# Kernel optimization log

Measured on AMD Instinct MI355X. Metric: run time of the kernel, lower is better.

## Reference

```python
import jax, jax.numpy as jnp
import numpy as np
import math

C = 1024
H = 16
D = C // H
R = 4  # max_relative_position (window_size)


def setup_inputs() -> dict:
    key = jax.random.key(0)
    ks = jax.random.split(key, 10)
    B, S = 2, 2048
    scale = 1.0 / math.sqrt(C)
    inp = {
        "x": jax.random.normal(ks[0], (B, S, C), dtype=jnp.float32),
        "mask": jnp.ones((B, 1, 1, S), dtype=jnp.int32),
        "Wq": jax.random.normal(ks[1], (C, C), dtype=jnp.float32) * scale,
        "bq": jnp.zeros((C,), dtype=jnp.float32),
        "Wk": jax.random.normal(ks[2], (C, C), dtype=jnp.float32) * scale,
        "bk": jnp.zeros((C,), dtype=jnp.float32),
        "Wv": jax.random.normal(ks[3], (C, C), dtype=jnp.float32) * scale,
        "bv": jnp.zeros((C,), dtype=jnp.float32),
        "Wo": jax.random.normal(ks[4], (C, C), dtype=jnp.float32) * scale,
        "bo": jnp.zeros((C,), dtype=jnp.float32),
        "rel_key": jax.random.normal(ks[5], (2 * R + 1, D), dtype=jnp.float32) * 0.02,
    }
    return inp


def reference(x, mask, Wq, bq, Wk, bk, Wv, bv, Wo, bo, rel_key):
    B, S, Cc = x.shape
    inv = 1.0 / math.sqrt(D)
    # projections -> [B, H, S, D]
    q = (x @ Wq.T + bq).reshape(B, S, H, D).transpose(0, 2, 1, 3)
    k = (x @ Wk.T + bk).reshape(B, S, H, D).transpose(0, 2, 1, 3)
    v = (x @ Wv.T + bv).reshape(B, S, H, D).transpose(0, 2, 1, 3)
    scores = jnp.einsum("bhqd,bhkd->bhqk", q, k) * inv
    # relative position bias: positions[q,k] in [0, 2R]
    pos = jnp.clip(jnp.arange(S)[None, :] - jnp.arange(S)[:, None], -R, R) + R
    # project q onto the small rel table first ([B,H,S,2R+1]), then gather per (q,k)
    proj = jnp.einsum("bhqd,rd->bhqr", q, rel_key) * inv
    rel_scores = proj[:, :, jnp.arange(S)[:, None], pos]  # [B,H,S,S]
    scores = scores + rel_scores
    scores = jnp.where(mask == 0, jnp.float32(-1e9), scores)
    attn = jax.nn.softmax(scores, axis=-1)
    out = jnp.einsum("bhqk,bhkd->bhqd", attn, v)
    out = out.transpose(0, 2, 1, 3).reshape(B, S, Cc)
    return out @ Wo.T + bo
```

## Files before the change

kernel.cpp:

```cpp
#include <hip/hip_runtime.h>

#define B_ 2
#define S_ 2048
#define C_ 1024
#define H_ 16
#define D_ 64

typedef _Float16 f16;
typedef _Float16 half8 __attribute__((ext_vector_type(8)));
typedef _Float16 half4v __attribute__((ext_vector_type(4)));
typedef float floatx4 __attribute__((ext_vector_type(4)));

#define LD4F(p) (*reinterpret_cast<const float4*>(p))
#define LD16U(p) (*reinterpret_cast<const uint4*>(p))
#define EXP2F(x) __builtin_amdgcn_exp2f(x)

__device__ __forceinline__ void gload16(const f16* g, f16* l) {
    __builtin_amdgcn_global_load_lds(
        (const __attribute__((address_space(1))) void*)g,
        (__attribute__((address_space(3))) void*)l, 16, 0, 0);
}

__global__ __launch_bounds__(256)
void convert_inputs(const float* __restrict__ x,
                    const float* __restrict__ Wq, const float* __restrict__ Wk,
                    const float* __restrict__ Wv, const float* __restrict__ Wo,
                    f16* __restrict__ dst)
{
    const size_t XN = (size_t)B_ * S_ * C_;
    const size_t WN = (size_t)C_ * C_;
    size_t i = (size_t)blockIdx.x * 256 + threadIdx.x;
    size_t e = i * 4;
    if (e >= XN + 4 * WN) return;
    const float* s; size_t o;
    if (e < XN) { s = x; o = e; }
    else {
        size_t j = e - XN;
        int w = (int)(j >> 20);
        s = (w == 0) ? Wq : (w == 1) ? Wk : (w == 2) ? Wv : Wo;
        o = j & (WN - 1);
    }
    float4 val = LD4F(&s[o]);
    half4v hv;
    hv[0] = (f16)val.x; hv[1] = (f16)val.y; hv[2] = (f16)val.z; hv[3] = (f16)val.w;
    *reinterpret_cast<half4v*>(&dst[e]) = hv;
}

__global__ __launch_bounds__(256)
void qkv_gemm_h(const f16* __restrict__ xh, const f16* __restrict__ Wbase,
                const float* __restrict__ bq, const float* __restrict__ bk,
                const float* __restrict__ bv,
                f16* __restrict__ qo, f16* __restrict__ ko, f16* __restrict__ vo)
{
    const int which = blockIdx.z;
    const f16* W      = Wbase + (size_t)which * C_ * C_;
    const float* bias = (which == 0) ? bq : (which == 1) ? bk : bv;
    f16* out          = (which == 0) ? qo : (which == 1) ? ko : vo;
    const float qscale = (which == 0) ? 0.18033688f : 1.0f;

    const int mb = blockIdx.x * 128;
    const int nb = blockIdx.y * 128;
    const int tid = threadIdx.x;
    const int lane = tid & 63;
    const int wid = tid >> 6;
    const int wr = wid >> 1, wc = wid & 1;
    const int l15 = lane & 15, g = lane >> 4;

    __shared__ __align__(16) f16 As[128 * 32];
    __shared__ __align__(16) f16 Bs[128 * 32];

    floatx4 acc[4][4];
#pragma unroll
    for (int m = 0; m < 4; ++m)
#pragma unroll
        for (int n = 0; n < 4; ++n) acc[m][n] = (floatx4){0.f, 0.f, 0.f, 0.f};

    for (int k0 = 0; k0 < C_; k0 += 32) {
        __syncthreads();
#pragma unroll
        for (int p = 0; p < 2; ++p) {
            int i2 = tid + 256 * p;
            int row = i2 >> 2, c4 = i2 & 3;
            gload16(&xh[(size_t)(mb + row) * C_ + k0 + c4 * 8], &As[i2 * 8]);
            gload16(&W [(size_t)(nb + row) * C_ + k0 + c4 * 8], &Bs[i2 * 8]);
        }
        __syncthreads();

        half8 af[4];
#pragma unroll
        for (int m = 0; m < 4; ++m)
            af[m] = *reinterpret_cast<const half8*>(&As[(wr * 64 + m * 16 + l15) * 32 + g * 8]);
#pragma unroll
        for (int n = 0; n < 4; ++n) {
            half8 bf = *reinterpret_cast<const half8*>(&Bs[(wc * 64 + n * 16 + l15) * 32 + g * 8]);
#pragma unroll
            for (int m = 0; m < 4; ++m)
                acc[m][n] = __builtin_amdgcn_mfma_f32_16x16x32_f16(af[m], bf, acc[m][n], 0, 0, 0);
        }
    }

#pragma unroll
    for (int n = 0; n < 4; ++n) {
        int col = nb + wc * 64 + n * 16 + l15;
        float bb = bias[col];
        int h = col >> 6, d = col & 63;
#pragma unroll
        for (int m = 0; m < 4; ++m)
#pragma unroll
            for (int r = 0; r < 4; ++r) {
                int row = mb + wr * 64 + m * 16 + g * 4 + r;
                int b = row >> 11, s = row & (S_ - 1);
                out[(((size_t)b * H_ + h) * S_ + s) * D_ + d] = (f16)((acc[m][n][r] + bb) * qscale);
            }
    }
}

__global__ __launch_bounds__(256)
void attn_mfma(const f16* __restrict__ q, const f16* __restrict__ k,
               const f16* __restrict__ v, const int* __restrict__ mask,
               const float* __restrict__ rel, f16* __restrict__ ctx)
{
    const int flat = blockIdx.y * 32 + blockIdx.x;
    const int c = flat & 7, j = flat >> 3;
    const int bh = (c << 2) | (j >> 5);
    const int qb = (j & 31) * 64;

    const int b = bh >> 4, h = bh & 15;
    const f16* qh_ = q + (size_t)bh * S_ * D_;
    const f16* kh_ = k + (size_t)bh * S_ * D_;
    const f16* vh_ = v + (size_t)bh * S_ * D_;

    const int tid = threadIdx.x;
    const int lane = tid & 63;
    const int wid = tid >> 6;
    const int l15 = lane & 15, g = lane >> 4;

    __shared__ __align__(16) f16 Ks[64 * 72];
    __shared__ __align__(16) f16 Vt[64 * 72];
    __shared__ __align__(16) f16 Ps[4][16 * 72];
    __shared__ float Prj[64][12];

    const int qrow = qb + wid * 16 + l15;
    half8 aq0 = *reinterpret_cast<const half8*>(&qh_[(size_t)qrow * D_ + g * 8]);
    half8 aq1 = *reinterpret_cast<const half8*>(&qh_[(size_t)qrow * D_ + 32 + g * 8]);

#pragma unroll
    for (int rr = 0; rr < 9; ++rr) {
        float p = 0.f;
#pragma unroll
        for (int jj = 0; jj < 8; ++jj) {
            p += (float)aq0[jj] * rel[rr * D_ + g * 8 + jj];
            p += (float)aq1[jj] * rel[rr * D_ + 32 + g * 8 + jj];
        }
        p += __shfl_xor(p, 16);
        p += __shfl_xor(p, 32);
        if (lane < 16) Prj[wid * 16 + l15][rr] = p;
    }

    float prj_lo[4], prj_hi[4];
#pragma unroll
    for (int r = 0; r < 4; ++r) {
        prj_lo[r] = Prj[wid * 16 + g * 4 + r][0];
        prj_hi[r] = Prj[wid * 16 + g * 4 + r][8];
    }

    floatx4 o[4];
    float mrun[4], lrun[4];
#pragma unroll
    for (int n = 0; n < 4; ++n) o[n] = (floatx4){0.f, 0.f, 0.f, 0.f};
#pragma unroll
    for (int r = 0; r < 4; ++r) { mrun[r] = -INFINITY; lrun[r] = 0.f; }

    for (int jt = 0; jt < S_ / 64; ++jt) {
        const int jb = jt * 64;
        uint4 kr[2], vr[2];
#pragma unroll
        for (int p = 0; p < 2; ++p) {
            int idx = tid + 256 * p;
            int row = idx >> 3, c8 = idx & 7;
            kr[p] = LD16U(&kh_[(size_t)(jb + row) * D_ + c8 * 8]);
            vr[p] = LD16U(&vh_[(size_t)(jb + row) * D_ + c8 * 8]);
        }
        __syncthreads();
#pragma unroll
        for (int p = 0; p < 2; ++p) {
            int idx = tid + 256 * p;
            int row = idx >> 3, c8 = idx & 7;
            *reinterpret_cast<uint4*>(&Ks[row * 72 + c8 * 8]) = kr[p];
            const f16* vp = reinterpret_cast<const f16*>(&vr[p]);
#pragma unroll
            for (int jj = 0; jj < 8; ++jj) {
                int dd = (jj + c8) & 7;
                Vt[(c8 * 8 + dd) * 72 + row] = vp[dd];
            }
        }
        __syncthreads();

        floatx4 sc[4];
#pragma unroll
        for (int n = 0; n < 4; ++n) sc[n] = (floatx4){0.f, 0.f, 0.f, 0.f};
#pragma unroll
        for (int n = 0; n < 4; ++n) {
            half8 bk0 = *reinterpret_cast<const half8*>(&Ks[(n * 16 + l15) * 72 + g * 8]);
            half8 bk1 = *reinterpret_cast<const half8*>(&Ks[(n * 16 + l15) * 72 + 32 + g * 8]);
            sc[n] = __builtin_amdgcn_mfma_f32_16x16x32_f16(aq0, bk0, sc[n], 0, 0, 0);
            sc[n] = __builtin_amdgcn_mfma_f32_16x16x32_f16(aq1, bk1, sc[n], 0, 0, 0);
        }

        float pvv[4][4];
        const bool diag = (jb >= qb - 64) && (jb <= qb + 64);
        if (!diag) {
            const float* pb = (jb > qb) ? prj_hi : prj_lo;
#pragma unroll
            for (int n = 0; n < 4; ++n) {
                int mv = mask[b * S_ + jb + n * 16 + l15];
#pragma unroll
                for (int r = 0; r < 4; ++r)
                    pvv[n][r] = mv ? (sc[n][r] + pb[r]) : -1.0e9f;
            }
        } else {
#pragma unroll
            for (int n = 0; n < 4; ++n) {
                int jg = jb + n * 16 + l15;
                int mv = mask[b * S_ + jg];
#pragma unroll
                for (int r = 0; r < 4; ++r) {
                    int ig = qb + wid * 16 + g * 4 + r;
                    int dp = jg - ig;
                    dp = dp < -4 ? -4 : (dp > 4 ? 4 : dp);
                    float val = sc[n][r] + Prj[wid * 16 + g * 4 + r][dp + 4];
                    pvv[n][r] = mv ? val : -1.0e9f;
                }
            }
        }

#pragma unroll
        for (int r = 0; r < 4; ++r) {
            float mx = fmaxf(fmaxf(pvv[0][r], pvv[1][r]), fmaxf(pvv[2][r], pvv[3][r]));
            mx = fmaxf(mx, __shfl_xor(mx, 1));
            mx = fmaxf(mx, __shfl_xor(mx, 2));
            mx = fmaxf(mx, __shfl_xor(mx, 4));
            mx = fmaxf(mx, __shfl_xor(mx, 8));
            float mnew = fmaxf(mrun[r], mx);
            float scl = EXP2F(mrun[r] - mnew);
            float rs = 0.f;
#pragma unroll
            for (int n = 0; n < 4; ++n) {
                float e = EXP2F(pvv[n][r] - mnew);
                pvv[n][r] = e; rs += e;
            }
            rs += __shfl_xor(rs, 1); rs += __shfl_xor(rs, 2);
            rs += __shfl_xor(rs, 4); rs += __shfl_xor(rs, 8);
            lrun[r] = lrun[r] * scl + rs;
            mrun[r] = mnew;
#pragma unroll
            for (int n = 0; n < 4; ++n) o[n][r] *= scl;
        }

#pragma unroll
        for (int n = 0; n < 4; ++n)
#pragma unroll
            for (int r = 0; r < 4; ++r)
                Ps[wid][(g * 4 + r) * 72 + n * 16 + l15] = (f16)pvv[n][r];

        half8 pa0 = *reinterpret_cast<const half8*>(&Ps[wid][l15 * 72 + g * 8]);
        half8 pa1 = *reinterpret_cast<const half8*>(&Ps[wid][l15 * 72 + 32 + g * 8]);

#pragma unroll
        for (int n = 0; n < 4; ++n) {
            half8 bv0 = *reinterpret_cast<const half8*>(&Vt[(n * 16 + l15) * 72 + g * 8]);
            half8 bv1 = *reinterpret_cast<const half8*>(&Vt[(n * 16 + l15) * 72 + 32 + g * 8]);
            o[n] = __builtin_amdgcn_mfma_f32_16x16x32_f16(pa0, bv0, o[n], 0, 0, 0);
            o[n] = __builtin_amdgcn_mfma_f32_16x16x32_f16(pa1, bv1, o[n], 0, 0, 0);
        }
    }

#pragma unroll
    for (int n = 0; n < 4; ++n) {
        int dcol = n * 16 + l15;
#pragma unroll
        for (int r = 0; r < 4; ++r) {
            int srow = qb + wid * 16 + g * 4 + r;
            float val = o[n][r] / lrun[r];
            ctx[((size_t)(b * S_ + srow)) * C_ + h * D_ + dcol] = (f16)val;
        }
    }
}

__global__ __launch_bounds__(256)
void out_gemm_h(const f16* __restrict__ A, const f16* __restrict__ W,
                const float* __restrict__ bias, float* __restrict__ out)
{
    const int mb = blockIdx.x * 128;
    const int nb = blockIdx.y * 128;
    const int tid = threadIdx.x;
    const int lane = tid & 63;
    const int wid = tid >> 6;
    const int wr = wid >> 1, wc = wid & 1;
    const int l15 = lane & 15, g = lane >> 4;

    __shared__ __align__(16) f16 As[128 * 32];
    __shared__ __align__(16) f16 Bs[128 * 32];

    floatx4 acc[4][4];
#pragma unroll
    for (int m = 0; m < 4; ++m)
#pragma unroll
        for (int n = 0; n < 4; ++n) acc[m][n] = (floatx4){0.f, 0.f, 0.f, 0.f};

    for (int k0 = 0; k0 < C_; k0 += 32) {
        __syncthreads();
#pragma unroll
        for (int p = 0; p < 2; ++p) {
            int i2 = tid + 256 * p;
            int row = i2 >> 2, c4 = i2 & 3;
            gload16(&A[(size_t)(mb + row) * C_ + k0 + c4 * 8], &As[i2 * 8]);
            gload16(&W[(size_t)(nb + row) * C_ + k0 + c4 * 8], &Bs[i2 * 8]);
        }
        __syncthreads();

        half8 af[4];
#pragma unroll
        for (int m = 0; m < 4; ++m)
            af[m] = *reinterpret_cast<const half8*>(&As[(wr * 64 + m * 16 + l15) * 32 + g * 8]);
#pragma unroll
        for (int n = 0; n < 4; ++n) {
            half8 bf = *reinterpret_cast<const half8*>(&Bs[(wc * 64 + n * 16 + l15) * 32 + g * 8]);
#pragma unroll
            for (int m = 0; m < 4; ++m)
                acc[m][n] = __builtin_amdgcn_mfma_f32_16x16x32_f16(af[m], bf, acc[m][n], 0, 0, 0);
        }
    }

#pragma unroll
    for (int n = 0; n < 4; ++n) {
        int col = nb + wc * 64 + n * 16 + l15;
        float bb = bias[col];
#pragma unroll
        for (int m = 0; m < 4; ++m)
#pragma unroll
            for (int r = 0; r < 4; ++r) {
                size_t row = mb + wr * 64 + m * 16 + g * 4 + r;
                out[row * C_ + col] = acc[m][n][r] + bb;
            }
    }
}

extern "C" void kernel_launch(void* const* d_in, const int* in_sizes, int n_in,
                              void* d_out, int out_size, void* d_ws, size_t ws_size,
                              hipStream_t stream)
{
    const float* x    = (const float*)d_in[0];
    const int*   mask = (const int*)  d_in[1];
    const float* Wq   = (const float*)d_in[2];
    const float* bq   = (const float*)d_in[3];
    const float* Wk   = (const float*)d_in[4];
    const float* bk   = (const float*)d_in[5];
    const float* Wv   = (const float*)d_in[6];
    const float* bv   = (const float*)d_in[7];
    const float* Wo   = (const float*)d_in[8];
    const float* bo   = (const float*)d_in[9];
    const float* rel  = (const float*)d_in[10];
    float* out = (float*)d_out;

    const size_t XN = (size_t)B_ * S_ * C_;
    const size_t WN = (size_t)C_ * C_;

    f16* wsh  = (f16*)d_ws;
    f16* xh   = wsh;
    f16* Wqh  = wsh + XN;
    f16* Woh  = Wqh + 3 * WN;
    f16* qh   = wsh + XN + 4 * WN;
    f16* kh   = qh + XN;
    f16* vh   = kh + XN;
    f16* ctxh = vh + XN;

    convert_inputs<<<8192, 256, 0, stream>>>(x, Wq, Wk, Wv, Wo, wsh);
    qkv_gemm_h<<<dim3(32, 8, 3), 256, 0, stream>>>(xh, Wqh, bq, bk, bv, qh, kh, vh);
    attn_mfma<<<dim3(32, 32), 256, 0, stream>>>(qh, kh, vh, mask, rel, ctxh);
    out_gemm_h<<<dim3(32, 8), 256, 0, stream>>>(ctxh, Woh, bo, out);
}
```

Measured before the change: 388.5 us.

## Load K fragments directly from global and double-buffer transposed V in LDS

The attention kernel no longer stages K through shared memory: each wave reads its K MFMA operands straight from global memory into registers. V is double-buffered in LDS, with the next tile's global loads issued before the current tile's compute and written into the spare buffer afterwards. This cuts the loop from two block barriers per tile to one and overlaps V loading with compute. The trade-off is that every wave now fetches the same K tile separately through cache instead of sharing one LDS copy, which adds global/L2 traffic, and the V prefetch raises register pressure.

New measurement: 399.8 us. +2.9%, slower.

```diff
diff --git a/kernel.cpp b/kernel.cpp
--- a/kernel.cpp
+++ b/kernel.cpp
@@ -135,10 +135,12 @@
     const int wid = tid >> 6;
     const int l15 = lane & 15, g = lane >> 4;
 
-    __shared__ __align__(16) f16 Ks[64 * 72];
-    __shared__ __align__(16) f16 Vt[64 * 72];
+    __shared__ __align__(16) f16 Vt[2][64 * 72];
     __shared__ __align__(16) f16 Ps[4][16 * 72];
     __shared__ float Prj[64][12];
+
+    const int srow = tid >> 3;
+    const int sc8  = tid & 7;
 
     const int qrow = qb + wid * 16 + l15;
     half8 aq0 = *reinterpret_cast<const half8*>(&qh_[(size_t)qrow * D_ + g * 8]);
@@ -156,7 +158,6 @@
         p += __shfl_xor(p, 32);
         if (lane < 16) Prj[wid * 16 + l15][rr] = p;
     }
-
     float prj_lo[4], prj_hi[4];
 #pragma unroll
     for (int r = 0; r < 4; ++r) {
@@ -171,40 +172,47 @@
 #pragma unroll
     for (int r = 0; r < 4; ++r) { mrun[r] = -INFINITY; lrun[r] = 0.f; }
 
+    {
+        uint4 vr0 = LD16U(&vh_[(size_t)srow * D_ + sc8 * 8]);
+        uint4 vr1 = LD16U(&vh_[(size_t)(32 + srow) * D_ + sc8 * 8]);
+        const f16* vp0 = reinterpret_cast<const f16*>(&vr0);
+        const f16* vp1 = reinterpret_cast<const f16*>(&vr1);
+#pragma unroll
+        for (int jj = 0; jj < 8; ++jj) {
+            int dd = (jj + sc8) & 7;
+            Vt[0][(sc8 * 8 + dd) * 72 + srow]      = vp0[dd];
+            Vt[0][(sc8 * 8 + dd) * 72 + 32 + srow] = vp1[dd];
+        }
+    }
+    __syncthreads();
+
     for (int jt = 0; jt < S_ / 64; ++jt) {
         const int jb = jt * 64;
-        uint4 kr[2], vr[2];
-#pragma unroll
-        for (int p = 0; p < 2; ++p) {
-            int idx = tid + 256 * p;
-            int row = idx >> 3, c8 = idx & 7;
-            kr[p] = LD16U(&kh_[(size_t)(jb + row) * D_ + c8 * 8]);
-            vr[p] = LD16U(&vh_[(size_t)(jb + row) * D_ + c8 * 8]);
-        }
-        __syncthreads();
-#pragma unroll
-        for (int p = 0; p < 2; ++p) {
-            int idx = tid + 256 * p;
-            int row = idx >> 3, c8 = idx & 7;
-            *reinterpret_cast<uint4*>(&Ks[row * 72 + c8 * 8]) = kr[p];
-            const f16* vp = reinterpret_cast<const f16*>(&vr[p]);
-#pragma unroll
-            for (int jj = 0; jj < 8; ++jj) {
-                int dd = (jj + c8) & 7;
-                Vt[(c8 * 8 + dd) * 72 + row] = vp[dd];
-            }
-        }
-        __syncthreads();
+        const int cur = jt & 1, nxt = cur ^ 1;
+
+        uint4 vr0, vr1;
+        const bool pf = (jt + 1 < S_ / 64);
+        if (pf) {
+            const int jb2 = jb + 64;
+            vr0 = LD16U(&vh_[(size_t)(jb2 + srow) * D_ + sc8 * 8]);
+            vr1 = LD16U(&vh_[(size_t)(jb2 + 32 + srow) * D_ + sc8 * 8]);
+        }
+
+        half8 kf0[4], kf1[4];
+#pragma unroll
+        for (int n = 0; n < 4; ++n) {
+            const f16* kp = &kh_[(size_t)(jb + n * 16 + l15) * D_ + g * 8];
+            kf0[n] = *reinterpret_cast<const half8*>(kp);
+            kf1[n] = *reinterpret_cast<const half8*>(kp + 32);
+        }
 
         floatx4 sc[4];
 #pragma unroll
         for (int n = 0; n < 4; ++n) sc[n] = (floatx4){0.f, 0.f, 0.f, 0.f};
 #pragma unroll
         for (int n = 0; n < 4; ++n) {
-            half8 bk0 = *reinterpret_cast<const half8*>(&Ks[(n * 16 + l15) * 72 + g * 8]);
-            half8 bk1 = *reinterpret_cast<const half8*>(&Ks[(n * 16 + l15) * 72 + 32 + g * 8]);
-            sc[n] = __builtin_amdgcn_mfma_f32_16x16x32_f16(aq0, bk0, sc[n], 0, 0, 0);
-            sc[n] = __builtin_amdgcn_mfma_f32_16x16x32_f16(aq1, bk1, sc[n], 0, 0, 0);
+            sc[n] = __builtin_amdgcn_mfma_f32_16x16x32_f16(aq0, kf0[n], sc[n], 0, 0, 0);
+            sc[n] = __builtin_amdgcn_mfma_f32_16x16x32_f16(aq1, kf1[n], sc[n], 0, 0, 0);
         }
 
         float pvv[4][4];
@@ -268,11 +276,23 @@
 
 #pragma unroll
         for (int n = 0; n < 4; ++n) {
-            half8 bv0 = *reinterpret_cast<const half8*>(&Vt[(n * 16 + l15) * 72 + g * 8]);
-            half8 bv1 = *reinterpret_cast<const half8*>(&Vt[(n * 16 + l15) * 72 + 32 + g * 8]);
+            half8 bv0 = *reinterpret_cast<const half8*>(&Vt[cur][(n * 16 + l15) * 72 + g * 8]);
+            half8 bv1 = *reinterpret_cast<const half8*>(&Vt[cur][(n * 16 + l15) * 72 + 32 + g * 8]);
             o[n] = __builtin_amdgcn_mfma_f32_16x16x32_f16(pa0, bv0, o[n], 0, 0, 0);
             o[n] = __builtin_amdgcn_mfma_f32_16x16x32_f16(pa1, bv1, o[n], 0, 0, 0);
         }
+
+        if (pf) {
+            const f16* vp0 = reinterpret_cast<const f16*>(&vr0);
+            const f16* vp1 = reinterpret_cast<const f16*>(&vr1);
+#pragma unroll
+            for (int jj = 0; jj < 8; ++jj) {
+                int dd = (jj + sc8) & 7;
+                Vt[nxt][(sc8 * 8 + dd) * 72 + srow]      = vp0[dd];
+                Vt[nxt][(sc8 * 8 + dd) * 72 + 32 + srow] = vp1[dd];
+            }
+        }
+        __syncthreads();
     }
 
 #pragma unroll
@@ -280,9 +300,9 @@
         int dcol = n * 16 + l15;
 #pragma unroll
         for (int r = 0; r < 4; ++r) {
-            int srow = qb + wid * 16 + g * 4 + r;
+            int srow2 = qb + wid * 16 + g * 4 + r;
             float val = o[n][r] / lrun[r];
-            ctx[((size_t)(b * S_ + srow)) * C_ + h * D_ + dcol] = (f16)val;
+            ctx[((size_t)(b * S_ + srow2)) * C_ + h * D_ + dcol] = (f16)val;
         }
     }
 }
```
